# Kernel tuning notes

Hardware: AMD Instinct MI355X
Metric: run time of the kernel (lower is better)

Reference implementation:

```python
import jax, jax.numpy as jnp
import numpy as np

C = 64
K = 3          # kernel_size
EK = 5         # encoder_kernel
PAD = (K - 1) // 2


def _conv(x, w, pad):
    return jax.lax.conv_general_dilated(
        x, w, window_strides=(1, 1), padding=[(pad, pad), (pad, pad)],
        dimension_numbers=('NCHW', 'OIHW', 'NCHW'))


def setup_inputs() -> dict:
    key = jax.random.key(0)
    ks = jax.random.split(key, 6)
    b, h, w = 8, 128, 128
    x = jax.random.normal(ks[0], (b, C, h, w), dtype=jnp.float32)
    # gen_kernel: 1x1 conv (C->C, with bias) then EKxEK conv (C->K*K, no bias)
    w1 = jax.random.normal(ks[1], (C, C, 1, 1), dtype=jnp.float32) * (1.0 / np.sqrt(C))
    b1 = jax.random.normal(ks[2], (C,), dtype=jnp.float32) * 0.01
    w2 = jax.random.normal(ks[3], (K * K, C, EK, EK), dtype=jnp.float32) * (1.0 / np.sqrt(C * EK * EK))
    # consensus t_c: 1x1 conv C->C//4, relu, 1x1 conv C//4->C, relu (no bias)
    tc1 = jax.random.normal(ks[4], (C // 4, C, 1, 1), dtype=jnp.float32) * (1.0 / np.sqrt(C))
    tc2 = jax.random.normal(ks[5], (C, C // 4, 1, 1), dtype=jnp.float32) * (1.0 / np.sqrt(C // 4))
    return {"x": x, "w1": w1, "b1": b1, "w2": w2, "tc1": tc1, "tc2": tc2}


def reference(x, w1, b1, w2, tc1, tc2):
    b, c, h, w = x.shape
    oh, ow = h, w  # stride == 1
    # dynamic kernel logits: (b, K*K, oh, ow)
    y = _conv(x, w1, 0) + b1[None, :, None, None]
    wt = _conv(y, w2, (EK - 1) // 2)
    # consensus scale: adaptive avg pool to 1x1 then mean over batch -> (c,)
    x_con = jnp.mean(x, axis=(0, 2, 3))                      # (c,)
    h1 = jax.nn.relu(jnp.einsum('oc,c->o', tc1[:, :, 0, 0], x_con))
    tmp = jax.nn.relu(jnp.einsum('oc,c->o', tc2[:, :, 0, 0], h1))  # (c,)
    # broadcast logits to (b, c, K*K, oh, ow) and softmax over K*K
    logits = wt[:, None, :, :, :] * tmp[None, :, None, None, None]
    attn = jax.nn.softmax(logits, axis=2)                    # (b,c,9,oh,ow)
    # unfold patches: reflect-pad then 9 shifted views, order kh*K+kw (row-major)
    px = jnp.pad(x, ((0, 0), (0, 0), (PAD, PAD), (PAD, PAD)), mode='reflect')
    pats = jnp.stack([px[:, :, i:i + oh, j:j + ow]
                      for i in range(K) for j in range(K)], axis=2)  # (b,c,9,oh,ow)
    out = jnp.sum(attn * pats, axis=2)                       # (b,c,oh,ow)
    return out
```

## Files before the change

kernel.cpp:

```cpp
#include <hip/hip_runtime.h>
#include <hip/hip_bf16.h>
#include <cstddef>


#define B 8
#define C 64
#define HW 128
#define NK 9
#define NT 25
#define XR 132
#define LOG2E 1.4426950408889634f

typedef __attribute__((ext_vector_type(8))) short short8;
typedef __attribute__((ext_vector_type(4))) float float4v;
typedef __attribute__((ext_vector_type(4))) unsigned int uint4v;

__device__ __forceinline__ unsigned short f2bf(float f) {
    unsigned int u = __float_as_uint(f);
    unsigned int r = u + 0x7FFF + ((u >> 16) & 1);
    return (unsigned short)(r >> 16);
}
__device__ __forceinline__ float fast_exp2(float x) {
    float r;
    asm("v_exp_f32 %0, %1" : "=v"(r) : "v"(x));
    return r;
}
__device__ __forceinline__ float fast_rcp(float x) {
    float r;
    asm("v_rcp_f32 %0, %1" : "=v"(r) : "v"(x));
    return r;
}
__device__ __forceinline__ void load_lds16(const unsigned short* g, unsigned short* l) {
    __builtin_amdgcn_global_load_lds(
        (const __attribute__((address_space(1))) unsigned int*)g,
        (__attribute__((address_space(3))) unsigned int*)l,
        16, 0, 0);
}

__global__ __launch_bounds__(256) void xcon_kernel(const float* __restrict__ x,
                                                   float* __restrict__ part) {
    const int c = blockIdx.x >> 2, qb = blockIdx.x & 3;
    float s = 0.f;
    for (int bb = 0; bb < 2; ++bb) {
        const int b = qb * 2 + bb;
        const float4* p = (const float4*)(x + ((size_t)(b * C + c)) * (HW * HW));
        for (int idx = threadIdx.x; idx < (HW * HW) / 4; idx += 256) {
            float4 v = p[idx];
            s += (v.x + v.y) + (v.z + v.w);
        }
    }
    __shared__ float red[256];
    red[threadIdx.x] = s;
    __syncthreads();
    for (int off = 128; off > 0; off >>= 1) {
        if (threadIdx.x < off) red[threadIdx.x] += red[threadIdx.x + off];
        __syncthreads();
    }
    if (threadIdx.x == 0) part[c * 4 + qb] = red[0];
}

__global__ __launch_bounds__(256) void xpack_kernel(const float* __restrict__ x,
                                                    unsigned short* __restrict__ xbf) {
    const int r = blockIdx.x, b = blockIdx.y;
    unsigned short* rowp = xbf + ((size_t)(b * XR + r)) * (XR * 64);
    const int t = threadIdx.x;
    if (r < 2 || r >= 130) {
        const uint4v z = {0u, 0u, 0u, 0u};
        for (int idx = t; idx < 1056; idx += 256)
            *(uint4v*)(rowp + idx * 8) = z;
        return;
    }
    const int h = r - 2;
    if (t < 32) {
        const uint4v z = {0u, 0u, 0u, 0u};
        const int q4 = t & 3;
        const int wc = (q4 < 2) ? q4 : (q4 + 128);
        *(uint4v*)(rowp + wc * 64 + ((t >> 2) << 3)) = z;
    }
    const int c8 = t >> 5;
    const int wl = t & 31;
    const float* xp = x + (((size_t)(b * C + c8 * 8)) * HW + h) * HW;
#pragma unroll
    for (int k = 0; k < 4; ++k) {
        const int gw = wl + 32 * k;
        const int wc = gw + 2;
        uint4v dv;
#pragma unroll
        for (int j = 0; j < 4; ++j) {
            const float v0 = xp[(size_t)(2 * j) * (HW * HW) + gw];
            const float v1 = xp[(size_t)(2 * j + 1) * (HW * HW) + gw];
            dv[j] = (unsigned int)f2bf(v0) | ((unsigned int)f2bf(v1) << 16);
        }
        const int sw = ((r & 1) * 4 + wc) & 7;
        *(uint4v*)(rowp + wc * 64 + ((c8 ^ sw) << 3)) = dv;
    }
}

__global__ __launch_bounds__(256) void prep_kernel(const float* __restrict__ w1,
                                                   const float* __restrict__ b1,
                                                   const float* __restrict__ w2,
                                                   unsigned short* __restrict__ Abuf,
                                                   float* __restrict__ betaG) {
    if (blockIdx.x < 50) {
        __shared__ float sw2[NK * 64];
        __shared__ float sw1[64 * 32];
        const int chunk = blockIdx.x;
        const int t = chunk >> 1, ch = chunk & 1;
        for (int idx = threadIdx.x; idx < NK * 64; idx += 256) {
            const int m = idx >> 6, cc = idx & 63;
            sw2[idx] = w2[(m * 64 + cc) * NT + t];
        }
        for (int idx = threadIdx.x; idx < 2048; idx += 256) {
            const int cc = idx >> 5, j = idx & 31;
            sw1[idx] = w1[cc * 64 + ch * 32 + j];
        }
        __syncthreads();
        for (int sidx = 0; sidx < 2; ++sidx) {
            const int slot = sidx * 256 + threadIdx.x;
            const int quad = slot >> 7, m = (slot >> 3) & 15, jj = slot & 7;
            unsigned short hi = 0, lo = 0;
            if (m < NK) {
                float s = 0.f;
                for (int cc = 0; cc < 64; ++cc)
                    s += sw2[m * 64 + cc] * sw1[cc * 32 + quad * 8 + jj];
                hi = f2bf(s);
                lo = f2bf(s - __uint_as_float(((unsigned int)hi) << 16));
            }
            Abuf[chunk * 1024 + slot] = hi;
            Abuf[chunk * 1024 + 512 + slot] = lo;
        }
    } else {
        __shared__ float beta_s[NT * NK];
        const int t0 = threadIdx.x;
        if (t0 < NT * NK) {
            const int t = t0 / NK, k = t0 - t * NK;
            float s = 0.f;
            for (int cc = 0; cc < 64; ++cc)
                s += w2[(k * 64 + cc) * NT + t] * b1[cc];
            beta_s[t0] = s;
        }
        __syncthreads();
        if (t0 < 225) {
            const int ic = t0 / 45, jc = (t0 / 9) % 5, k = t0 % 9;
            float s = 0.f;
            for (int eh = 0; eh < 5; ++eh) {
                bool rok = (ic == 0) ? (eh >= 2) : (ic == 1) ? (eh >= 1)
                          : (ic == 3) ? (eh <= 3) : (ic == 4) ? (eh <= 2) : true;
                if (!rok) continue;
                for (int ew = 0; ew < 5; ++ew) {
                    bool cok = (jc == 0) ? (ew >= 2) : (jc == 1) ? (ew >= 1)
                              : (jc == 3) ? (ew <= 3) : (jc == 4) ? (ew <= 2) : true;
                    if (cok) s += beta_s[(eh * 5 + ew) * NK + k];
                }
            }
            betaG[t0] = s;
        }
    }
}

__global__ __launch_bounds__(512, 4) void fused_kernel(const unsigned short* __restrict__ xbf,
                                                       const unsigned short* __restrict__ Abuf,
                                                       const float* __restrict__ betaG,
                                                       const float* __restrict__ part,
                                                       const float* __restrict__ tc1,
                                                       const float* __restrict__ tc2,
                                                       float* __restrict__ out) {
    __shared__ __align__(16) unsigned short stag[400 * 64];
    __shared__ float wpart[128 * 10];
    __shared__ float lt[C];
    const int b = blockIdx.y;
    const int i0 = (blockIdx.x >> 3) * 16, j0 = (blockIdx.x & 7) * 16;
    const int tid = threadIdx.x, lane = tid & 63, wid = tid >> 6;
    const int n = lane & 15, q = lane >> 4;
    const int rowg = wid >> 1, h = wid & 1;

    {
        const unsigned short* xrow0 = xbf + (((size_t)(b * XR + i0)) * XR + j0) * 64;
#pragma unroll
        for (int k = 0; k < 6; ++k) {
            const int ci = k * 512 + tid;
            const int li = ((ci >> 5) * 205) >> 10;
            const int rem = ci - li * 160;
            load_lds16(xrow0 + li * (XR * 64) + rem * 8, stag + ci * 8);
        }
        if (tid < 128) {
            const int ci = 3072 + tid;
            const int li = ((ci >> 5) * 205) >> 10;
            const int rem = ci - li * 160;
            load_lds16(xrow0 + li * (XR * 64) + rem * 8, stag + ci * 8);
        }
    }

    if (wid == 0) {
        float xcv = (part[lane * 4 + 0] + part[lane * 4 + 1]
                   + part[lane * 4 + 2] + part[lane * 4 + 3]) * (1.f / (B * HW * HW));
        float hh = 0.f;
        for (int c = 0; c < C; ++c) {
            float xcc = __shfl(xcv, c);
            if (lane < 16) hh += tc1[lane * C + c] * xcc;
        }
        hh = fmaxf(hh, 0.f);
        float ltv = 0.f;
#pragma unroll
        for (int o = 0; o < 16; ++o) {
            float ho = __shfl(hh, o);
            ltv += tc2[lane * 16 + o] * ho;
        }
        lt[lane] = fmaxf(ltv, 0.f) * LOG2E;
    }

    const int prow = rowg * 4 + q;
    const int pgi = i0 + prow, pgj = j0 + n;
    float bgv[NK];
    if (h == 0) {
        const int ic = pgi < 2 ? pgi : (pgi > 125 ? pgi - 123 : 2);
        const int jc = pgj < 2 ? pgj : (pgj > 125 ? pgj - 123 : 2);
        const float* bp = betaG + (ic * 5 + jc) * NK;
#pragma unroll
        for (int k = 0; k < NK; ++k) bgv[k] = bp[k];
    }

    __syncthreads();

    float4v acc[4];
    const float4v zero4 = {0.f, 0.f, 0.f, 0.f};
#pragma unroll
    for (int g = 0; g < 4; ++g) acc[g] = zero4;

    const unsigned short* Ab = Abuf + h * 1024 + lane * 8;
    const int chs = (h << 2) | q;
    const int rb = rowg * 4;
#pragma unroll
    for (int ew = 0; ew < 5; ++ew) {
        short8 w8[8];
#pragma unroll
        for (int rr = 0; rr < 8; ++rr) {
            const int px = (rb + rr) * 20 + ew + n;
            w8[rr] = *(const short8*)(stag + px * 64 + ((chs ^ (px & 7)) << 3));
        }
#pragma unroll
        for (int eh = 0; eh < 5; ++eh) {
            const int t = eh * 5 + ew;
            const short8 ahi = *(const short8*)(Ab + t * 2048);
            const short8 alo = *(const short8*)(Ab + t * 2048 + 512);
#pragma unroll
            for (int g = 0; g < 4; ++g) {
                acc[g] = __builtin_amdgcn_mfma_f32_16x16x32_bf16(ahi, w8[g + eh], acc[g], 0, 0, 0);
                acc[g] = __builtin_amdgcn_mfma_f32_16x16x32_bf16(alo, w8[g + eh], acc[g], 0, 0, 0);
            }
        }
    }

    float wv[NK];
#pragma unroll
    for (int k = 0; k < NK; ++k) {
        const int src = (k >> 2) * 16 + n;
        const int rr = k & 3;
        float v0 = __shfl(acc[0][rr], src);
        float v1 = __shfl(acc[1][rr], src);
        float v2 = __shfl(acc[2][rr], src);
        float v3 = __shfl(acc[3][rr], src);
        wv[k] = (q == 0) ? v0 : (q == 1) ? v1 : (q == 2) ? v2 : v3;
    }

    const int lp = ((rowg & 1) << 6) + lane;
    for (int pg = 0; pg < 2; ++pg) {
        const bool inpass = (rowg >> 1) == pg;
        if (pg) __syncthreads();
        if (inpass && h == 1) {
#pragma unroll
            for (int k = 0; k < NK; ++k) wpart[lp * 10 + k] = wv[k];
        }
        __syncthreads();
        if (inpass && h == 0) {
            float w9[NK];
            float wmax = -1e30f;
#pragma unroll
            for (int k = 0; k < NK; ++k) {
                w9[k] = wv[k] + wpart[lp * 10 + k] + bgv[k];
                wmax = fmaxf(wmax, w9[k]);
            }
#pragma unroll
            for (int k = 0; k < NK; ++k) wpart[lp * 10 + k] = w9[k] - wmax;
        }
        __syncthreads();
#pragma unroll
        for (int s = 0; s < 2; ++s) {
            const int task = tid * 2 + s;
            const int lpx = task >> 3, oct = task & 7;
            const int l6 = lpx & 63;
            const int brow = (2 * pg + (lpx >> 6)) * 4 + (l6 >> 4);
            const int bcol = l6 & 15;
            const int bgi = i0 + brow, bgj = j0 + bcol;
            float dv[NK];
#pragma unroll
            for (int k = 0; k < NK; ++k) dv[k] = wpart[lpx * 10 + k];
            int r0 = bgi - 1; r0 = r0 < 0 ? 1 : r0;
            int r2 = bgi + 1; r2 = r2 > 127 ? 126 : r2;
            int c0 = bgj - 1; c0 = c0 < 0 ? 1 : c0;
            int c2 = bgj + 1; c2 = c2 > 127 ? 126 : c2;
            const int R[3] = {r0 - i0 + 2, bgi - i0 + 2, r2 - i0 + 2};
            const int Cc[3] = {c0 - j0 + 2, bgj - j0 + 2, c2 - j0 + 2};
            uint4v xs[NK];
#pragma unroll
            for (int kh = 0; kh < 3; ++kh)
#pragma unroll
                for (int kw = 0; kw < 3; ++kw) {
                    const int prc = R[kh] * 20 + Cc[kw];
                    xs[kh * 3 + kw] = *(const uint4v*)(stag + prc * 64 + ((oct ^ (prc & 7)) << 3));
                }
            float* outp = out + (((size_t)b * C + oct * 8) * HW + bgi) * HW + bgj;
#pragma unroll
            for (int jj = 0; jj < 4; ++jj) {
                const float t0 = lt[oct * 8 + jj * 2];
                const float t1 = lt[oct * 8 + jj * 2 + 1];
                float s0 = 0.f, o0 = 0.f, s1 = 0.f, o1 = 0.f;
#pragma unroll
                for (int k = 0; k < NK; ++k) {
                    const unsigned int u = xs[k][jj];
                    const float e0 = fast_exp2(dv[k] * t0);
                    const float e1 = fast_exp2(dv[k] * t1);
                    s0 += e0; o0 = fmaf(e0, __uint_as_float(u << 16), o0);
                    s1 += e1; o1 = fmaf(e1, __uint_as_float(u & 0xffff0000u), o1);
                }
                outp[(size_t)(jj * 2) * (HW * HW)] = o0 * fast_rcp(s0);
                outp[(size_t)(jj * 2 + 1) * (HW * HW)] = o1 * fast_rcp(s1);
            }
        }
    }
}

extern "C" void kernel_launch(void* const* d_in, const int* in_sizes, int n_in,
                              void* d_out, int out_size, void* d_ws, size_t ws_size,
                              hipStream_t stream) {
    const float* x   = (const float*)d_in[0];
    const float* w1  = (const float*)d_in[1];
    const float* b1  = (const float*)d_in[2];
    const float* w2  = (const float*)d_in[3];
    const float* tc1 = (const float*)d_in[4];
    const float* tc2 = (const float*)d_in[5];
    float* out = (float*)d_out;

    char* ws = (char*)d_ws;
    float* part  = (float*)(ws + 0);
    unsigned short* Abuf = (unsigned short*)(ws + 1024);
    float* betaG = (float*)(ws + 103424);
    unsigned short* xbf  = (unsigned short*)(ws + 104448);

    xcon_kernel<<<256, 256, 0, stream>>>(x, part);
    xpack_kernel<<<dim3(XR, B), 256, 0, stream>>>(x, xbf);
    prep_kernel<<<51, 256, 0, stream>>>(w1, b1, w2, Abuf, betaG);
    fused_kernel<<<dim3(64, B), 512, 0, stream>>>(xbf, Abuf, betaG, part, tc1, tc2, out);
}
```

Measured before the change: 146.6 us.

## Fuse channel-mean reduction into bf16 pack kernel and shrink fused tile

Drops the separate xcon kernel, which read all of x a second time. Per-row channel sums are now computed inside xpack_kernel while it already reads x, then reduced by an extra prep_kernel block. The fused kernel moves from 16x16 tiles with 512 threads to 8x16 tiles with 256 threads, doubling the block count and cutting LDS staging per block. The trade-off is an extra workspace buffer and more halo rows reloaded for the smaller tiles.

```diff
diff --git a/kernel.cpp b/kernel.cpp
--- a/kernel.cpp
+++ b/kernel.cpp
@@ -9,6 +9,10 @@
 #define NK 9
 #define NT 25
 #define XR 132
+#define TI 8
+#define TJ 16
+#define HR 12
+#define HC 20
 #define LOG2E 1.4426950408889634f
 
 typedef __attribute__((ext_vector_type(8))) short short8;
@@ -37,30 +41,9 @@
         16, 0, 0);
 }
 
-__global__ __launch_bounds__(256) void xcon_kernel(const float* __restrict__ x,
-                                                   float* __restrict__ part) {
-    const int c = blockIdx.x >> 2, qb = blockIdx.x & 3;
-    float s = 0.f;
-    for (int bb = 0; bb < 2; ++bb) {
-        const int b = qb * 2 + bb;
-        const float4* p = (const float4*)(x + ((size_t)(b * C + c)) * (HW * HW));
-        for (int idx = threadIdx.x; idx < (HW * HW) / 4; idx += 256) {
-            float4 v = p[idx];
-            s += (v.x + v.y) + (v.z + v.w);
-        }
-    }
-    __shared__ float red[256];
-    red[threadIdx.x] = s;
-    __syncthreads();
-    for (int off = 128; off > 0; off >>= 1) {
-        if (threadIdx.x < off) red[threadIdx.x] += red[threadIdx.x + off];
-        __syncthreads();
-    }
-    if (threadIdx.x == 0) part[c * 4 + qb] = red[0];
-}
-
 __global__ __launch_bounds__(256) void xpack_kernel(const float* __restrict__ x,
-                                                    unsigned short* __restrict__ xbf) {
+                                                    unsigned short* __restrict__ xbf,
+                                                    float* __restrict__ part_rows) {
     const int r = blockIdx.x, b = blockIdx.y;
     unsigned short* rowp = xbf + ((size_t)(b * XR + r)) * (XR * 64);
     const int t = threadIdx.x;
@@ -80,6 +63,7 @@
     const int c8 = t >> 5;
     const int wl = t & 31;
     const float* xp = x + (((size_t)(b * C + c8 * 8)) * HW + h) * HW;
+    float s8[8] = {0.f, 0.f, 0.f, 0.f, 0.f, 0.f, 0.f, 0.f};
 #pragma unroll
     for (int k = 0; k < 4; ++k) {
         const int gw = wl + 32 * k;
@@ -89,18 +73,32 @@
         for (int j = 0; j < 4; ++j) {
             const float v0 = xp[(size_t)(2 * j) * (HW * HW) + gw];
             const float v1 = xp[(size_t)(2 * j + 1) * (HW * HW) + gw];
+            s8[2 * j] += v0;
+            s8[2 * j + 1] += v1;
             dv[j] = (unsigned int)f2bf(v0) | ((unsigned int)f2bf(v1) << 16);
         }
         const int sw = ((r & 1) * 4 + wc) & 7;
         *(uint4v*)(rowp + wc * 64 + ((c8 ^ sw) << 3)) = dv;
+    }
+#pragma unroll
+    for (int off = 16; off > 0; off >>= 1) {
+#pragma unroll
+        for (int j = 0; j < 8; ++j) s8[j] += __shfl_down(s8[j], off);
+    }
+    if (wl == 0) {
+        float* pr = part_rows + ((size_t)(b * HW + h)) * 64 + c8 * 8;
+#pragma unroll
+        for (int j = 0; j < 8; ++j) pr[j] = s8[j];
     }
 }
 
 __global__ __launch_bounds__(256) void prep_kernel(const float* __restrict__ w1,
                                                    const float* __restrict__ b1,
                                                    const float* __restrict__ w2,
+                                                   const float* __restrict__ part_rows,
                                                    unsigned short* __restrict__ Abuf,
-                                                   float* __restrict__ betaG) {
+                                                   float* __restrict__ betaG,
+                                                   float* __restrict__ part) {
     if (blockIdx.x < 50) {
         __shared__ float sw2[NK * 64];
         __shared__ float sw1[64 * 32];
@@ -129,7 +127,7 @@
             Abuf[chunk * 1024 + slot] = hi;
             Abuf[chunk * 1024 + 512 + slot] = lo;
         }
-    } else {
+    } else if (blockIdx.x == 50) {
         __shared__ float beta_s[NT * NK];
         const int t0 = threadIdx.x;
         if (t0 < NT * NK) {
@@ -155,21 +153,33 @@
             }
             betaG[t0] = s;
         }
-    }
-}
-
-__global__ __launch_bounds__(512, 4) void fused_kernel(const unsigned short* __restrict__ xbf,
+    } else {
+        const int c = threadIdx.x >> 2, seg = threadIdx.x & 3;
+        const float* pr = part_rows + (size_t)(seg * 256) * 64 + c;
+        float s0 = 0.f, s1 = 0.f, s2 = 0.f, s3 = 0.f;
+#pragma unroll 4
+        for (int i = 0; i < 256; i += 4) {
+            s0 += pr[(size_t)(i + 0) * 64];
+            s1 += pr[(size_t)(i + 1) * 64];
+            s2 += pr[(size_t)(i + 2) * 64];
+            s3 += pr[(size_t)(i + 3) * 64];
+        }
+        part[c * 4 + seg] = (s0 + s1) + (s2 + s3);
+    }
+}
+
+__global__ __launch_bounds__(256, 4) void fused_kernel(const unsigned short* __restrict__ xbf,
                                                        const unsigned short* __restrict__ Abuf,
                                                        const float* __restrict__ betaG,
                                                        const float* __restrict__ part,
                                                        const float* __restrict__ tc1,
                                                        const float* __restrict__ tc2,
                                                        float* __restrict__ out) {
-    __shared__ __align__(16) unsigned short stag[400 * 64];
-    __shared__ float wpart[128 * 10];
+    __shared__ __align__(16) unsigned short stag[HR * HC * 64];
+    __shared__ float wpart[128 * 9];
     __shared__ float lt[C];
     const int b = blockIdx.y;
-    const int i0 = (blockIdx.x >> 3) * 16, j0 = (blockIdx.x & 7) * 16;
+    const int i0 = (blockIdx.x >> 3) * TI, j0 = (blockIdx.x & 7) * TJ;
     const int tid = threadIdx.x, lane = tid & 63, wid = tid >> 6;
     const int n = lane & 15, q = lane >> 4;
     const int rowg = wid >> 1, h = wid & 1;
@@ -177,14 +187,14 @@
     {
         const unsigned short* xrow0 = xbf + (((size_t)(b * XR + i0)) * XR + j0) * 64;
 #pragma unroll
-        for (int k = 0; k < 6; ++k) {
-            const int ci = k * 512 + tid;
+        for (int k = 0; k < 7; ++k) {
+            const int ci = k * 256 + tid;
             const int li = ((ci >> 5) * 205) >> 10;
             const int rem = ci - li * 160;
             load_lds16(xrow0 + li * (XR * 64) + rem * 8, stag + ci * 8);
         }
         if (tid < 128) {
-            const int ci = 3072 + tid;
+            const int ci = 1792 + tid;
             const int li = ((ci >> 5) * 205) >> 10;
             const int rem = ci - li * 160;
             load_lds16(xrow0 + li * (XR * 64) + rem * 8, stag + ci * 8);
@@ -235,7 +245,7 @@
         short8 w8[8];
 #pragma unroll
         for (int rr = 0; rr < 8; ++rr) {
-            const int px = (rb + rr) * 20 + ew + n;
+            const int px = (rb + rr) * HC + ew + n;
             w8[rr] = *(const short8*)(stag + px * 64 + ((chs ^ (px & 7)) << 3));
         }
 #pragma unroll
@@ -263,50 +273,48 @@
         wv[k] = (q == 0) ? v0 : (q == 1) ? v1 : (q == 2) ? v2 : v3;
     }
 
-    const int lp = ((rowg & 1) << 6) + lane;
-    for (int pg = 0; pg < 2; ++pg) {
-        const bool inpass = (rowg >> 1) == pg;
-        if (pg) __syncthreads();
-        if (inpass && h == 1) {
-#pragma unroll
-            for (int k = 0; k < NK; ++k) wpart[lp * 10 + k] = wv[k];
-        }
-        __syncthreads();
-        if (inpass && h == 0) {
-            float w9[NK];
-            float wmax = -1e30f;
-#pragma unroll
-            for (int k = 0; k < NK; ++k) {
-                w9[k] = wv[k] + wpart[lp * 10 + k] + bgv[k];
-                wmax = fmaxf(wmax, w9[k]);
-            }
-#pragma unroll
-            for (int k = 0; k < NK; ++k) wpart[lp * 10 + k] = w9[k] - wmax;
-        }
-        __syncthreads();
-#pragma unroll
-        for (int s = 0; s < 2; ++s) {
-            const int task = tid * 2 + s;
-            const int lpx = task >> 3, oct = task & 7;
-            const int l6 = lpx & 63;
-            const int brow = (2 * pg + (lpx >> 6)) * 4 + (l6 >> 4);
-            const int bcol = l6 & 15;
-            const int bgi = i0 + brow, bgj = j0 + bcol;
-            float dv[NK];
-#pragma unroll
-            for (int k = 0; k < NK; ++k) dv[k] = wpart[lpx * 10 + k];
-            int r0 = bgi - 1; r0 = r0 < 0 ? 1 : r0;
-            int r2 = bgi + 1; r2 = r2 > 127 ? 126 : r2;
-            int c0 = bgj - 1; c0 = c0 < 0 ? 1 : c0;
-            int c2 = bgj + 1; c2 = c2 > 127 ? 126 : c2;
-            const int R[3] = {r0 - i0 + 2, bgi - i0 + 2, r2 - i0 + 2};
-            const int Cc[3] = {c0 - j0 + 2, bgj - j0 + 2, c2 - j0 + 2};
+    const int slot = rowg * 64 + lane;
+    if (h == 1) {
+#pragma unroll
+        for (int k = 0; k < NK; ++k) wpart[slot * 9 + k] = wv[k];
+    }
+    __syncthreads();
+    if (h == 0) {
+        float w9[NK];
+        float wmax = -1e30f;
+#pragma unroll
+        for (int k = 0; k < NK; ++k) {
+            w9[k] = wv[k] + wpart[slot * 9 + k] + bgv[k];
+            wmax = fmaxf(wmax, w9[k]);
+        }
+#pragma unroll
+        for (int k = 0; k < NK; ++k) wpart[slot * 9 + k] = w9[k] - wmax;
+    }
+    __syncthreads();
+
+#pragma unroll
+    for (int sp = 0; sp < 2; ++sp) {
+        const int lpx = lane + (sp << 6);
+        const int brow = lpx >> 4, bcol = lpx & 15;
+        const int bgi = i0 + brow, bgj = j0 + bcol;
+        float dv[NK];
+#pragma unroll
+        for (int k = 0; k < NK; ++k) dv[k] = wpart[lpx * 9 + k];
+        int r0 = bgi - 1; r0 = r0 < 0 ? 1 : r0;
+        int r2 = bgi + 1; r2 = r2 > 127 ? 126 : r2;
+        int c0 = bgj - 1; c0 = c0 < 0 ? 1 : c0;
+        int c2 = bgj + 1; c2 = c2 > 127 ? 126 : c2;
+        const int R[3] = {r0 - i0 + 2, bgi - i0 + 2, r2 - i0 + 2};
+        const int Cc[3] = {c0 - j0 + 2, bgj - j0 + 2, c2 - j0 + 2};
+#pragma unroll
+        for (int oc = 0; oc < 2; ++oc) {
+            const int oct = wid * 2 + oc;
             uint4v xs[NK];
 #pragma unroll
             for (int kh = 0; kh < 3; ++kh)
 #pragma unroll
                 for (int kw = 0; kw < 3; ++kw) {
-                    const int prc = R[kh] * 20 + Cc[kw];
+                    const int prc = R[kh] * HC + Cc[kw];
                     xs[kh * 3 + kw] = *(const uint4v*)(stag + prc * 64 + ((oct ^ (prc & 7)) << 3));
                 }
             float* outp = out + (((size_t)b * C + oct * 8) * HW + bgi) * HW + bgj;
@@ -345,10 +353,10 @@
     float* part  = (float*)(ws + 0);
     unsigned short* Abuf = (unsigned short*)(ws + 1024);
     float* betaG = (float*)(ws + 103424);
-    unsigned short* xbf  = (unsigned short*)(ws + 104448);
-
-    xcon_kernel<<<256, 256, 0, stream>>>(x, part);
-    xpack_kernel<<<dim3(XR, B), 256, 0, stream>>>(x, xbf);
-    prep_kernel<<<51, 256, 0, stream>>>(w1, b1, w2, Abuf, betaG);
-    fused_kernel<<<dim3(64, B), 512, 0, stream>>>(xbf, Abuf, betaG, part, tc1, tc2, out);
-}
+    float* part_rows = (float*)(ws + 104448);
+    unsigned short* xbf  = (unsigned short*)(ws + 366592);
+
+    xpack_kernel<<<dim3(XR, B), 256, 0, stream>>>(x, xbf, part_rows);
+    prep_kernel<<<52, 256, 0, stream>>>(w1, b1, w2, part_rows, Abuf, betaG, part);
+    fused_kernel<<<dim3(128, B), 256, 0, stream>>>(xbf, Abuf, betaG, part, tc1, tc2, out);
+}
```

Measured after the change: 132.1 us. 1.11x faster.
